# Kernel tuning notes

Hardware: AMD Instinct MI355X
Metric: run time of the kernel (lower is better)

## Reference

```python
import jax, jax.numpy as jnp
import numpy as np

BETA = 0.25
EPS_NORM = 1e-12   # matches torch F.normalize eps
EPS_COS = 1e-6     # clamp floor for cos weight


def _l2_normalize(v, axis=-1):
    n = jnp.linalg.norm(v, axis=axis, keepdims=True)
    return v / jnp.maximum(n, EPS_NORM)


def setup_inputs() -> dict:
    key = jax.random.key(0)
    kx, kc = jax.random.split(key)
    x = jax.random.normal(kx, (64, 1024, 256), dtype=jnp.float32)
    codebook = jax.random.normal(kc, (4096, 256), dtype=jnp.float32)
    return {"x": x, "codebook": codebook}


def reference(x, codebook):
    # Normalize codebook rows (F.normalize(codebook, dim=-1)).
    cb_n = _l2_normalize(codebook)                     # [K, D]
    # Cosine distance: 1 - cos_sim(x, cb). Only sim matters for argmin.
    x_n = _l2_normalize(x)                             # [B, S, D]
    sim = jnp.einsum('bsd,kd->bsk', x_n, cb_n)         # [B, S, K]
    dists = 1.0 - sim
    ids = jnp.argmin(dists, axis=-1)                   # [B, S] int
    c_k = cb_n[ids]                                    # [B, S, D] gather
    # Cosine weight uses RAW x (x_norm = x in the torch code).
    cos_k = jnp.sum(x * c_k, axis=-1, keepdims=True)   # [B, S, 1]
    cos_k = jnp.maximum(cos_k, EPS_COS)
    weighted_emb = cos_k * c_k                         # [B, S, D]
    # Cosine quantization loss: codebook term + beta * commitment term,
    # each 1 - cos_sim with stop-gradient on the opposite operand.
    def cos_sim(a, b):
        return jnp.sum(_l2_normalize(a) * _l2_normalize(b), axis=-1)
    codebook_term = jnp.mean(1.0 - cos_sim(jax.lax.stop_gradient(x), c_k))
    commit_term = jnp.mean(1.0 - cos_sim(x, jax.lax.stop_gradient(c_k)))
    loss = codebook_term + BETA * commit_term
    return ids, weighted_emb, loss
```

## Files before the change

kernel.cpp:

```cpp
#include <hip/hip_runtime.h>
#include <math.h>
#include <stdint.h>


#define TOKENS 65536
#define DIM 256
#define KCB 4096

#define TB 64
#define DELTA_SCALE 0.03125f
#define LIST_CAP (1u << 21)
#define SCAP 4096

typedef short bf16x8 __attribute__((ext_vector_type(8)));
typedef float f32x4 __attribute__((ext_vector_type(4)));

__device__ inline short f2bf(float f) {
    uint32_t u = __float_as_uint(f);
    u += 0x7FFF + ((u >> 16) & 1);
    return (short)(u >> 16);
}

__global__ void prep_all(const float* __restrict__ cb, const float* __restrict__ x,
                         float* __restrict__ cbn, short* __restrict__ cbh2,
                         float* __restrict__ xnorm, float* __restrict__ invnx) {
    int bid  = blockIdx.x;
    int w    = threadIdx.x >> 6;
    int lane = threadIdx.x & 63;
    if (bid < KCB / 4) {
        int row = bid * 4 + w;
        float4 v = *(const float4*)(cb + (size_t)row * DIM + lane * 4);
        float ss = v.x * v.x + v.y * v.y + v.z * v.z + v.w * v.w;
#pragma unroll
        for (int off = 32; off; off >>= 1) ss += __shfl_xor(ss, off);
        float scale = 1.0f / fmaxf(sqrtf(ss), 1e-12f);
        float4 o = {v.x * scale, v.y * scale, v.z * scale, v.w * scale};
        *(float4*)(cbn + (size_t)row * DIM + lane * 4) = o;
        short4 h = {f2bf(o.x), f2bf(o.y), f2bf(o.z), f2bf(o.w)};
        int g = row >> 4, l15 = row & 15;
        int kst = lane >> 3, q = (lane >> 1) & 3, jhalf = lane & 1;
        size_t dst = ((size_t)((g * 8 + kst) * 64 + q * 16 + l15)) * 8 + jhalf * 4;
        *(short4*)(cbh2 + dst) = h;
    } else {
        int row = (bid - KCB / 4) * 4 + w;
        float4 v = *(const float4*)(x + (size_t)row * DIM + lane * 4);
        float ss = v.x * v.x + v.y * v.y + v.z * v.z + v.w * v.w;
#pragma unroll
        for (int off = 32; off; off >>= 1) ss += __shfl_xor(ss, off);
        if (lane == 0) {
            float n = fmaxf(sqrtf(ss), 1e-12f);
            xnorm[row] = n;
            invnx[row] = 1.0f / n;
        }
    }
}

__global__ __launch_bounds__(256, 2) void mfma_select(
    const float* __restrict__ x, const short* __restrict__ cbh2,
    const float* __restrict__ xnorm,
    uint32_t* __restrict__ list, uint32_t* __restrict__ cnt) {
    __shared__ uint32_t s_list[SCAP];
    __shared__ uint32_t s_cnt, s_base;
    __shared__ float maxbuf[4][TB];

    const int tid  = threadIdx.x;
    const int lane = tid & 63;
    const int wn   = tid >> 6;
    const int l15  = lane & 15, q = lane >> 4;
    const int tb   = blockIdx.x * TB;

    if (tid == 0) s_cnt = 0;

    bf16x8 areg[4][8];
#pragma unroll
    for (int mf = 0; mf < 4; ++mf) {
        const float* xr = x + (size_t)(tb + mf * 16 + l15) * DIM + q * 8;
#pragma unroll
        for (int kst = 0; kst < 8; ++kst) {
            float4 f0 = *(const float4*)(xr + kst * 32);
            float4 f1 = *(const float4*)(xr + kst * 32 + 4);
            bf16x8 h;
            h[0] = f2bf(f0.x); h[1] = f2bf(f0.y); h[2] = f2bf(f0.z); h[3] = f2bf(f0.w);
            h[4] = f2bf(f1.x); h[5] = f2bf(f1.y); h[6] = f2bf(f1.z); h[7] = f2bf(f1.w);
            areg[mf][kst] = h;
        }
    }

    float rmax[4][4];
#pragma unroll
    for (int mf = 0; mf < 4; ++mf)
#pragma unroll
        for (int r = 0; r < 4; ++r) rmax[mf][r] = -3.0e38f;

    for (int ct = 0; ct < 32; ++ct) {
        const short* bp = cbh2 + (size_t)(wn * 64 + ct * 2) * 4096 + lane * 8;
        bf16x8 b[16];
#pragma unroll
        for (int j = 0; j < 8; ++j) {
            b[j]     = *(const bf16x8*)(bp + j * 512);
            b[j + 8] = *(const bf16x8*)(bp + 4096 + j * 512);
        }
        f32x4 acc[4][2];
#pragma unroll
        for (int mf = 0; mf < 4; ++mf)
#pragma unroll
            for (int nf = 0; nf < 2; ++nf) acc[mf][nf] = (f32x4){0.f, 0.f, 0.f, 0.f};
#pragma unroll
        for (int kst = 0; kst < 8; ++kst)
#pragma unroll
            for (int mf = 0; mf < 4; ++mf) {
                acc[mf][0] = __builtin_amdgcn_mfma_f32_16x16x32_bf16(areg[mf][kst], b[kst], acc[mf][0], 0, 0, 0);
                acc[mf][1] = __builtin_amdgcn_mfma_f32_16x16x32_bf16(areg[mf][kst], b[kst + 8], acc[mf][1], 0, 0, 0);
            }
#pragma unroll
        for (int mf = 0; mf < 4; ++mf)
#pragma unroll
            for (int r = 0; r < 4; ++r)
                rmax[mf][r] = fmaxf(rmax[mf][r], fmaxf(acc[mf][0][r], acc[mf][1][r]));
    }

#pragma unroll
    for (int mf = 0; mf < 4; ++mf)
#pragma unroll
        for (int r = 0; r < 4; ++r) {
            float v = rmax[mf][r];
#pragma unroll
            for (int o = 1; o < 16; o <<= 1) v = fmaxf(v, __shfl_xor(v, o));
            rmax[mf][r] = v;
        }
    if (l15 == 0) {
#pragma unroll
        for (int mf = 0; mf < 4; ++mf)
#pragma unroll
            for (int r = 0; r < 4; ++r)
                maxbuf[wn][mf * 16 + q * 4 + r] = rmax[mf][r];
    }
    __syncthreads();
    float thr[4][4];
#pragma unroll
    for (int mf = 0; mf < 4; ++mf)
#pragma unroll
        for (int r = 0; r < 4; ++r) {
            int tl = mf * 16 + q * 4 + r;
            float m = fmaxf(fmaxf(maxbuf[0][tl], maxbuf[1][tl]),
                            fmaxf(maxbuf[2][tl], maxbuf[3][tl]));
            thr[mf][r] = m - DELTA_SCALE * xnorm[tb + tl];
        }

    for (int ct = 0; ct < 32; ++ct) {
        const short* bp = cbh2 + (size_t)(wn * 64 + ct * 2) * 4096 + lane * 8;
        bf16x8 b[16];
#pragma unroll
        for (int j = 0; j < 8; ++j) {
            b[j]     = *(const bf16x8*)(bp + j * 512);
            b[j + 8] = *(const bf16x8*)(bp + 4096 + j * 512);
        }
        f32x4 acc[4][2];
#pragma unroll
        for (int mf = 0; mf < 4; ++mf)
#pragma unroll
            for (int nf = 0; nf < 2; ++nf) acc[mf][nf] = (f32x4){0.f, 0.f, 0.f, 0.f};
#pragma unroll
        for (int kst = 0; kst < 8; ++kst)
#pragma unroll
            for (int mf = 0; mf < 4; ++mf) {
                acc[mf][0] = __builtin_amdgcn_mfma_f32_16x16x32_bf16(areg[mf][kst], b[kst], acc[mf][0], 0, 0, 0);
                acc[mf][1] = __builtin_amdgcn_mfma_f32_16x16x32_bf16(areg[mf][kst], b[kst + 8], acc[mf][1], 0, 0, 0);
            }
#pragma unroll
        for (int mf = 0; mf < 4; ++mf)
#pragma unroll
            for (int nf = 0; nf < 2; ++nf)
#pragma unroll
                for (int r = 0; r < 4; ++r) {
                    if (acc[mf][nf][r] >= thr[mf][r]) {
                        uint32_t t = tb + mf * 16 + q * 4 + r;
                        uint32_t c = wn * 1024 + ct * 32 + nf * 16 + l15;
                        uint32_t e = (t << 12) | c;
                        uint32_t idx = atomicAdd(&s_cnt, 1u);
                        if (idx < SCAP) {
                            s_list[idx] = e;
                        } else {
                            uint32_t g2 = atomicAdd(cnt, 1u);
                            if (g2 < LIST_CAP) list[g2] = e;
                        }
                    }
                }
    }

    __syncthreads();
    if (tid == 0) {
        uint32_t m = s_cnt;
        if (m > SCAP) m = SCAP;
        s_base = atomicAdd(cnt, m);
        s_cnt = m;
    }
    __syncthreads();
    for (uint32_t i = tid; i < s_cnt; i += 256) {
        uint32_t idx = s_base + i;
        if (idx < LIST_CAP) list[idx] = s_list[i];
    }
}

__global__ void rescore(const float* __restrict__ x, const float* __restrict__ cbn,
                        const float* __restrict__ invnx,
                        const uint32_t* __restrict__ list, const uint32_t* __restrict__ cnt,
                        unsigned long long* __restrict__ win) {
    uint32_t n = *cnt;
    if (n > LIST_CAP) n = LIST_CAP;
    for (uint32_t e = blockIdx.x * blockDim.x + threadIdx.x; e < n;
         e += gridDim.x * blockDim.x) {
        uint32_t v = list[e];
        uint32_t t = v >> 12, c = v & 4095;
        const float* xp = x + (size_t)t * DIM;
        const float* cp = cbn + (size_t)c * DIM;
        float acc = 0.0f;
#pragma unroll 8
        for (int k = 0; k < DIM; ++k) acc = fmaf(xp[k], cp[k], acc);
        float s = acc * invnx[t];
        float dist = 1.0f - s;
        uint32_t u = __float_as_uint(dist);
        u = (u & 0x80000000u) ? ~u : (u | 0x80000000u);
        unsigned long long key = ((unsigned long long)u << 32) | c;
        atomicMin(win + t, key);
    }
}

__global__ void epilogue_kernel(const float* __restrict__ x, const float* __restrict__ cbn,
                                const float* __restrict__ invnx,
                                const unsigned long long* __restrict__ win,
                                float* __restrict__ ids_f,
                                float* __restrict__ emb, float* __restrict__ partials) {
    int w    = threadIdx.x >> 6;
    int lane = threadIdx.x & 63;
    int t    = blockIdx.x * 4 + w;
    int id   = (int)(win[t] & 0xFFFFFFFFull);
    if ((unsigned)id > 4095u) id = 0;
    if (lane == 0) ids_f[t] = (float)id;

    float4 c4 = *(const float4*)(cbn + (size_t)id * DIM + lane * 4);
    float4 x4 = *(const float4*)(x + (size_t)t * DIM + lane * 4);
    float dxc = c4.x * x4.x + c4.y * x4.y + c4.z * x4.z + c4.w * x4.w;
    float ssc = c4.x * c4.x + c4.y * c4.y + c4.z * c4.z + c4.w * c4.w;
#pragma unroll
    for (int off = 32; off; off >>= 1) {
        dxc += __shfl_xor(dxc, off);
        ssc += __shfl_xor(ssc, off);
    }
    float cosk = fmaxf(dxc, 1e-6f);
    float4 o = {cosk * c4.x, cosk * c4.y, cosk * c4.z, cosk * c4.w};
    *(float4*)(emb + (size_t)t * DIM + lane * 4) = o;

    float invnc = 1.0f / fmaxf(sqrtf(ssc), 1e-12f);
    float term = 1.0f - dxc * invnx[t] * invnc;

    __shared__ float sterm[4];
    if (lane == 0) sterm[w] = term;
    __syncthreads();
    if (threadIdx.x == 0)
        partials[blockIdx.x] = sterm[0] + sterm[1] + sterm[2] + sterm[3];
}

__global__ void finalize_kernel(const float* __restrict__ partials, float* __restrict__ loss) {
    __shared__ float buf[256];
    float s = 0.0f;
    for (int i = threadIdx.x; i < TOKENS / 4; i += 256) s += partials[i];
    buf[threadIdx.x] = s;
    __syncthreads();
    for (int st = 128; st; st >>= 1) {
        if (threadIdx.x < st) buf[threadIdx.x] += buf[threadIdx.x + st];
        __syncthreads();
    }
    if (threadIdx.x == 0) loss[0] = buf[0] * (1.25f / (float)TOKENS);
}

extern "C" void kernel_launch(void* const* d_in, const int* in_sizes, int n_in,
                              void* d_out, int out_size, void* d_ws, size_t ws_size,
                              hipStream_t stream) {
    const float* x  = (const float*)d_in[0];
    const float* cb = (const float*)d_in[1];

    float* out   = (float*)d_out;
    float* ids_f = out;
    float* emb   = out + TOKENS;
    float* loss  = out + TOKENS + (size_t)TOKENS * DIM;

    float* ws = (float*)d_ws;
    float* cbn   = ws;
    short* cbh2  = (short*)(cbn + (size_t)KCB * DIM);
    float* xnorm = (float*)(cbh2 + (size_t)KCB * DIM);
    float* invnx = xnorm + TOKENS;
    unsigned long long* win = (unsigned long long*)(invnx + TOKENS);
    uint32_t* list = (uint32_t*)(win + TOKENS);
    uint32_t* cnt  = list + LIST_CAP;
    float* partials = (float*)(cnt + 16);

    hipMemsetAsync(cnt, 0, 64, stream);
    hipMemsetAsync(win, 0xFF, sizeof(unsigned long long) * TOKENS, stream);

    prep_all<<<KCB / 4 + TOKENS / 4, 256, 0, stream>>>(cb, x, cbn, cbh2, xnorm, invnx);
    mfma_select<<<TOKENS / TB, 256, 0, stream>>>(x, cbh2, xnorm, list, cnt);
    rescore<<<1024, 256, 0, stream>>>(x, cbn, invnx, list, cnt, win);
    epilogue_kernel<<<TOKENS / 4, 256, 0, stream>>>(x, cbn, invnx, win, ids_f, emb, partials);
    finalize_kernel<<<1, 256, 0, stream>>>(partials, loss);
}
```

Before: 465.8 us.

## Restructure MFMA select into 512-thread blocks splitting codebook halves across wave pairs

The select kernel now uses 512-thread blocks covering 256 tokens. Each wave handles 64 tokens against one half of the codebook (2048 codes), processing one 16-code fragment per iteration instead of two, and a scheduling barrier separates the B loads from the MFMAs. The goal is to cut per-wave register pressure (8 B fragments and 4 accumulators instead of 16 and 8) and to let wave pairs share codebook tiles through cache. The costs are more loop iterations with less independent MFMA work per load batch, and more tokens per block competing for the fixed 4096-entry shared candidate list, so more entries may spill to the global atomic path.

```diff
diff --git a/kernel.cpp b/kernel.cpp
--- a/kernel.cpp
+++ b/kernel.cpp
@@ -7,7 +7,7 @@
 #define DIM 256
 #define KCB 4096
 
-#define TB 64
+#define TB 256
 #define DELTA_SCALE 0.03125f
 #define LIST_CAP (1u << 21)
 #define SCAP 4096
@@ -55,26 +55,29 @@
     }
 }
 
-__global__ __launch_bounds__(256, 2) void mfma_select(
+__global__ __launch_bounds__(512, 2) void mfma_select(
     const float* __restrict__ x, const short* __restrict__ cbh2,
     const float* __restrict__ xnorm,
     uint32_t* __restrict__ list, uint32_t* __restrict__ cnt) {
     __shared__ uint32_t s_list[SCAP];
     __shared__ uint32_t s_cnt, s_base;
-    __shared__ float maxbuf[4][TB];
+    __shared__ float maxbuf[2][TB];
 
     const int tid  = threadIdx.x;
     const int lane = tid & 63;
-    const int wn   = tid >> 6;
+    const int wid  = tid >> 6;
+    const int tq   = wid >> 1;
+    const int ch   = wid & 1;
     const int l15  = lane & 15, q = lane >> 4;
     const int tb   = blockIdx.x * TB;
+    const int twb  = tb + tq * 64;
 
     if (tid == 0) s_cnt = 0;
 
     bf16x8 areg[4][8];
 #pragma unroll
     for (int mf = 0; mf < 4; ++mf) {
-        const float* xr = x + (size_t)(tb + mf * 16 + l15) * DIM + q * 8;
+        const float* xr = x + (size_t)(twb + mf * 16 + l15) * DIM + q * 8;
 #pragma unroll
         for (int kst = 0; kst < 8; ++kst) {
             float4 f0 = *(const float4*)(xr + kst * 32);
@@ -92,31 +95,26 @@
 #pragma unroll
         for (int r = 0; r < 4; ++r) rmax[mf][r] = -3.0e38f;
 
-    for (int ct = 0; ct < 32; ++ct) {
-        const short* bp = cbh2 + (size_t)(wn * 64 + ct * 2) * 4096 + lane * 8;
-        bf16x8 b[16];
-#pragma unroll
-        for (int j = 0; j < 8; ++j) {
-            b[j]     = *(const bf16x8*)(bp + j * 512);
-            b[j + 8] = *(const bf16x8*)(bp + 4096 + j * 512);
-        }
-        f32x4 acc[4][2];
+    for (int ct = 0; ct < 128; ++ct) {
+        const short* bp = cbh2 + (size_t)(ch * 128 + ct) * 4096 + lane * 8;
+        bf16x8 b[8];
+#pragma unroll
+        for (int j = 0; j < 8; ++j) b[j] = *(const bf16x8*)(bp + j * 512);
+        __builtin_amdgcn_sched_barrier(0);
+        f32x4 acc[4];
+#pragma unroll
+        for (int mf = 0; mf < 4; ++mf) acc[mf] = (f32x4){0.f, 0.f, 0.f, 0.f};
+#pragma unroll
+        for (int kst = 0; kst < 8; ++kst)
+#pragma unroll
+            for (int mf = 0; mf < 4; ++mf)
+                acc[mf] = __builtin_amdgcn_mfma_f32_16x16x32_bf16(
+                    areg[mf][kst], b[kst], acc[mf], 0, 0, 0);
 #pragma unroll
         for (int mf = 0; mf < 4; ++mf)
 #pragma unroll
-            for (int nf = 0; nf < 2; ++nf) acc[mf][nf] = (f32x4){0.f, 0.f, 0.f, 0.f};
-#pragma unroll
-        for (int kst = 0; kst < 8; ++kst)
-#pragma unroll
-            for (int mf = 0; mf < 4; ++mf) {
-                acc[mf][0] = __builtin_amdgcn_mfma_f32_16x16x32_bf16(areg[mf][kst], b[kst], acc[mf][0], 0, 0, 0);
-                acc[mf][1] = __builtin_amdgcn_mfma_f32_16x16x32_bf16(areg[mf][kst], b[kst + 8], acc[mf][1], 0, 0, 0);
-            }
-#pragma unroll
-        for (int mf = 0; mf < 4; ++mf)
-#pragma unroll
             for (int r = 0; r < 4; ++r)
-                rmax[mf][r] = fmaxf(rmax[mf][r], fmaxf(acc[mf][0][r], acc[mf][1][r]));
+                rmax[mf][r] = fmaxf(rmax[mf][r], acc[mf][r]);
     }
 
 #pragma unroll
@@ -133,7 +131,7 @@
         for (int mf = 0; mf < 4; ++mf)
 #pragma unroll
             for (int r = 0; r < 4; ++r)
-                maxbuf[wn][mf * 16 + q * 4 + r] = rmax[mf][r];
+                maxbuf[ch][tq * 64 + mf * 16 + q * 4 + r] = rmax[mf][r];
     }
     __syncthreads();
     float thr[4][4];
@@ -141,51 +139,43 @@
     for (int mf = 0; mf < 4; ++mf)
 #pragma unroll
         for (int r = 0; r < 4; ++r) {
-            int tl = mf * 16 + q * 4 + r;
-            float m = fmaxf(fmaxf(maxbuf[0][tl], maxbuf[1][tl]),
-                            fmaxf(maxbuf[2][tl], maxbuf[3][tl]));
-            thr[mf][r] = m - DELTA_SCALE * xnorm[tb + tl];
-        }
-
-    for (int ct = 0; ct < 32; ++ct) {
-        const short* bp = cbh2 + (size_t)(wn * 64 + ct * 2) * 4096 + lane * 8;
-        bf16x8 b[16];
-#pragma unroll
-        for (int j = 0; j < 8; ++j) {
-            b[j]     = *(const bf16x8*)(bp + j * 512);
-            b[j + 8] = *(const bf16x8*)(bp + 4096 + j * 512);
-        }
-        f32x4 acc[4][2];
+            int tl = tq * 64 + mf * 16 + q * 4 + r;
+            thr[mf][r] = fmaxf(maxbuf[0][tl], maxbuf[1][tl])
+                       - DELTA_SCALE * xnorm[tb + tl];
+        }
+
+    for (int ct = 0; ct < 128; ++ct) {
+        const short* bp = cbh2 + (size_t)(ch * 128 + ct) * 4096 + lane * 8;
+        bf16x8 b[8];
+#pragma unroll
+        for (int j = 0; j < 8; ++j) b[j] = *(const bf16x8*)(bp + j * 512);
+        __builtin_amdgcn_sched_barrier(0);
+        f32x4 acc[4];
+#pragma unroll
+        for (int mf = 0; mf < 4; ++mf) acc[mf] = (f32x4){0.f, 0.f, 0.f, 0.f};
+#pragma unroll
+        for (int kst = 0; kst < 8; ++kst)
+#pragma unroll
+            for (int mf = 0; mf < 4; ++mf)
+                acc[mf] = __builtin_amdgcn_mfma_f32_16x16x32_bf16(
+                    areg[mf][kst], b[kst], acc[mf], 0, 0, 0);
 #pragma unroll
         for (int mf = 0; mf < 4; ++mf)
 #pragma unroll
-            for (int nf = 0; nf < 2; ++nf) acc[mf][nf] = (f32x4){0.f, 0.f, 0.f, 0.f};
-#pragma unroll
-        for (int kst = 0; kst < 8; ++kst)
-#pragma unroll
-            for (int mf = 0; mf < 4; ++mf) {
-                acc[mf][0] = __builtin_amdgcn_mfma_f32_16x16x32_bf16(areg[mf][kst], b[kst], acc[mf][0], 0, 0, 0);
-                acc[mf][1] = __builtin_amdgcn_mfma_f32_16x16x32_bf16(areg[mf][kst], b[kst + 8], acc[mf][1], 0, 0, 0);
-            }
-#pragma unroll
-        for (int mf = 0; mf < 4; ++mf)
-#pragma unroll
-            for (int nf = 0; nf < 2; ++nf)
-#pragma unroll
-                for (int r = 0; r < 4; ++r) {
-                    if (acc[mf][nf][r] >= thr[mf][r]) {
-                        uint32_t t = tb + mf * 16 + q * 4 + r;
-                        uint32_t c = wn * 1024 + ct * 32 + nf * 16 + l15;
-                        uint32_t e = (t << 12) | c;
-                        uint32_t idx = atomicAdd(&s_cnt, 1u);
-                        if (idx < SCAP) {
-                            s_list[idx] = e;
-                        } else {
-                            uint32_t g2 = atomicAdd(cnt, 1u);
-                            if (g2 < LIST_CAP) list[g2] = e;
-                        }
+            for (int r = 0; r < 4; ++r) {
+                if (acc[mf][r] >= thr[mf][r]) {
+                    uint32_t t = twb + mf * 16 + q * 4 + r;
+                    uint32_t c = ch * 2048 + ct * 16 + l15;
+                    uint32_t e = (t << 12) | c;
+                    uint32_t idx = atomicAdd(&s_cnt, 1u);
+                    if (idx < SCAP) {
+                        s_list[idx] = e;
+                    } else {
+                        uint32_t g2 = atomicAdd(cnt, 1u);
+                        if (g2 < LIST_CAP) list[g2] = e;
                     }
                 }
+            }
     }
 
     __syncthreads();
@@ -196,7 +186,7 @@
         s_cnt = m;
     }
     __syncthreads();
-    for (uint32_t i = tid; i < s_cnt; i += 256) {
+    for (uint32_t i = tid; i < s_cnt; i += 512) {
         uint32_t idx = s_base + i;
         if (idx < LIST_CAP) list[idx] = s_list[i];
     }
@@ -299,7 +289,7 @@
     hipMemsetAsync(win, 0xFF, sizeof(unsigned long long) * TOKENS, stream);
 
     prep_all<<<KCB / 4 + TOKENS / 4, 256, 0, stream>>>(cb, x, cbn, cbh2, xnorm, invnx);
-    mfma_select<<<TOKENS / TB, 256, 0, stream>>>(x, cbh2, xnorm, list, cnt);
+    mfma_select<<<TOKENS / TB, 512, 0, stream>>>(x, cbh2, xnorm, list, cnt);
     rescore<<<1024, 256, 0, stream>>>(x, cbn, invnx, list, cnt, win);
     epilogue_kernel<<<TOKENS / 4, 256, 0, stream>>>(x, cbn, invnx, win, ids_f, emb, partials);
     finalize_kernel<<<1, 256, 0, stream>>>(partials, loss);
```

New measurement: 435.1 us. -6.6%, faster.
